# Kernel optimization log

Hardware: AMD Instinct MI355X
Metric: run time of the kernel (lower is better)

The kernel has to match this reference:

```python
import jax, jax.numpy as jnp
import numpy as np

B, T, I, H, K = 32, 1024, 512, 512, 2


def _causal_conv1d(x_bit, w_hik, b_h):
    # x_bit: [B, I, T]; left-pad K-1 zeros (ConstantPad1d((K-1, 0)))
    xp = jnp.pad(x_bit, ((0, 0), (0, 0), (K - 1, 0)))
    y = jax.lax.conv_general_dilated(
        xp, w_hik, window_strides=(1,), padding='VALID',
        dimension_numbers=('NCH', 'OIH', 'NCH'))  # [B, H, T]
    return y + b_h[None, :, None]


def setup_inputs() -> dict:
    key = jax.random.key(0)
    k1, k2, k3 = jax.random.split(key, 3)
    bound = 1.0 / np.sqrt(I * K)  # torch Conv1d default init scale
    return {
        'inputs': jax.random.normal(k1, (B, T, I), dtype=jnp.float32),
        'init_state': jnp.zeros((B, H), dtype=jnp.float32),
        'Wz': jax.random.uniform(k2, (H, I, K), jnp.float32, -bound, bound),
        'bz': jnp.zeros((H,), dtype=jnp.float32),
        'Wf': jax.random.uniform(k3, (H, I, K), jnp.float32, -bound, bound),
        'bf': jnp.zeros((H,), dtype=jnp.float32),
    }


def reference(inputs, init_state, Wz, bz, Wf, bf):
    # init_state is accepted but unused in the original forward (mode='f').
    x = inputs.transpose(0, 2, 1)                      # [B, I, T]
    raw_f = _causal_conv1d(x, Wf, bf).transpose(0, 2, 1)  # [B, T, H]
    raw_z = _causal_conv1d(x, Wz, bz).transpose(0, 2, 1)  # [B, T, H]

    log_f = jax.nn.log_sigmoid(raw_f)
    log_one_minus_f = jax.nn.log_sigmoid(-raw_f)
    log_z = jax.nn.log_sigmoid(raw_z)

    # recurrent_gates[t] = sum_{s>t} log_f[s]  (suffix sum of log_f over time, excluding t=0 shift)
    rg = log_f[:, 1:, :]                               # [B, T-1, H]
    cs = jnp.cumsum(rg, axis=1)
    rg = rg - cs + cs[:, -1:, :]
    rg = jnp.concatenate([rg, jnp.zeros((inputs.shape[0], 1, rg.shape[2]), dtype=rg.dtype)], axis=1)  # [B, T, H]

    log_hidden = jax.lax.cumlogsumexp(log_z + log_one_minus_f + rg, axis=1)
    hidden = jnp.exp(log_hidden - rg)
    return hidden
```

## Files before the change

kernel.cpp:

```cpp
#include <hip/hip_runtime.h>
#include <hip/hip_bf16.h>
#include <cstddef>
#include <cstdint>

#define B_  32
#define T_  1024
#define I_  512
#define H_  512
#define M_  (B_ * T_)
#define TP_ 1025

typedef __bf16 bf16x8  __attribute__((ext_vector_type(8)));
typedef float  floatx4 __attribute__((ext_vector_type(4)));
typedef unsigned short ushort8v __attribute__((ext_vector_type(8)));
typedef unsigned long long u64;

__device__ __forceinline__ unsigned short f2bf(float f) {
    uint32_t u = __float_as_uint(f);
    return (unsigned short)((u + 0x7FFFu + ((u >> 16) & 1u)) >> 16);
}
__device__ __forceinline__ float sigm(float x) {
    return __builtin_amdgcn_rcpf(1.f + __expf(-x));
}

#define GLL(src, dst) __builtin_amdgcn_global_load_lds( \
    (const __attribute__((address_space(1))) void*)(src), \
    (__attribute__((address_space(3))) void*)(dst), 16, 0, 0)

#define NB_BUILD 8200
#define NB_PACK  512
#define NB_ZERO  256

__global__ __launch_bounds__(256) void prep(const float* __restrict__ x,
                                            const float* __restrict__ Wf,
                                            const float* __restrict__ Wz,
                                            unsigned short* __restrict__ Ab2,
                                            unsigned short* __restrict__ Wq,
                                            uint4* __restrict__ HpubZ,
                                            uint32_t* __restrict__ tickets) {
    if (blockIdx.x < NB_BUILD) {
        int g = blockIdx.x * 256 + threadIdx.x;
        int idx8 = g << 3;
        int row = idx8 >> 9;
        int col = idx8 & 511;
        int b    = (int)((unsigned)row / TP_);
        int trow = row - b * TP_;
        ushort8v o = {0, 0, 0, 0, 0, 0, 0, 0};
        if (trow > 0) {
            const float* src = &x[((size_t)b * T_ + (trow - 1)) * I_ + col];
            float4 v0 = *(const float4*)src;
            float4 v1 = *(const float4*)(src + 4);
            o[0] = f2bf(v0.x); o[1] = f2bf(v0.y); o[2] = f2bf(v0.z); o[3] = f2bf(v0.w);
            o[4] = f2bf(v1.x); o[5] = f2bf(v1.y); o[6] = f2bf(v1.z); o[7] = f2bf(v1.w);
        }
        *(ushort8v*)&Ab2[(size_t)idx8] = o;
    } else if (blockIdx.x < NB_BUILD + NB_PACK) {
        int cid = (blockIdx.x - NB_BUILD) * 256 + threadIdx.x;
        int lane = cid & 63;
        int c    = (cid >> 6) & 3;
        int wn   = (cid >> 8) & 1;
        int ksub = (cid >> 9) & 31;
        int ni   = (cid >> 14) & 3;
        int gate = (cid >> 16) & 1;
        int n_col = ni * 128 + wn * 64 + c * 16 + (lane & 15);
        const float* G = gate ? Wz : Wf;
        ushort8v o;
        #pragma unroll
        for (int j = 0; j < 8; ++j) {
            int k   = ksub * 32 + (lane >> 4) * 8 + j;
            int tap = k >> 9;
            int i   = k & 511;
            o[j] = f2bf(G[n_col * (I_ * 2) + i * 2 + tap]);
        }
        *(ushort8v*)&Wq[(size_t)cid * 8] = o;
    } else {
        int g = (blockIdx.x - NB_BUILD - NB_PACK) * 256 + threadIdx.x;
        HpubZ[g] = make_uint4(0, 0, 0, 0);
        if (g < 256) tickets[g] = 0;
    }
}

__global__ __launch_bounds__(256, 3) void mfma_gemm_scan(
        const unsigned short* __restrict__ Ab2,
        const unsigned short* __restrict__ Wq,
        const float* __restrict__ biasF,
        const float* __restrict__ biasZ,
        float* __restrict__ out,
        u64* __restrict__ Hpub,
        uint32_t* __restrict__ tickets) {
    __shared__ unsigned short smem[12288];
    __shared__ uint32_t pos_s;

    const int tid = threadIdx.x;
    const int bid = blockIdx.x;
    const int x   = bid & 7;
    const int nh  = (bid >> 3) & 7;
    const int q   = bid >> 6;
    const int b   = ((q & 3) << 3) | x;
    const int chain = nh * 32 + b;
    if (tid == 0) pos_s = atomicAdd(&tickets[chain], 1u);
    __syncthreads();
    const int pos = (int)pos_s;
    const int h0  = nh * 64;
    const int browBase = b * TP_ + pos * 128;

    const int lane = tid & 63;
    const int wave = tid >> 6;
    const int wm   = wave >> 1;
    const int wh   = wave & 1;
    const int lm   = lane & 15, quad = lane >> 4;

    const int c0 = wave * 128 + lane;
    const int c1 = c0 + 64;
    const int r0 = c0 >> 2, q0 = (c0 & 3) ^ ((r0 >> 2) & 3);
    const int r1 = c1 >> 2, q1 = (c1 & 3) ^ ((r1 >> 2) & 3);

    const unsigned short* pA0 = Ab2 + (size_t)(browBase + r0) * 512 + q0 * 8;
    const unsigned short* pA1 = Ab2 + (size_t)(browBase + r1) * 512 + q1 * 8;

    const unsigned short* pBF = Wq + (size_t)(nh >> 1) * 131072
                                   + (nh & 1) * 2048 + wh * 1024 + lane * 8;

    int offA[4];
    #pragma unroll
    for (int r = 0; r < 4; ++r) {
        int ml = wm * 64 + r * 16 + lm;
        offA[r] = (4 * ml + (quad ^ ((ml >> 2) & 3))) * 8;
    }

    floatx4 accF[4][2] = {};
    floatx4 accZ[4][2] = {};
    bf16x8 bfA[2], bzA[2], bfB[2], bzB[2];

#define ISSUE_A(ksub, sA) do {                                          \
        const int aoff_ = (((ksub) >> 4) * 512) + (((ksub) & 15) * 32); \
        GLL(pA0 + aoff_, (sA) + wave * 1024);                           \
        GLL(pA1 + aoff_, (sA) + wave * 1024 + 512);                     \
    } while (0)

#define LOADB(ksub, BF, BZ) do {                                        \
        const unsigned short* pf_ = pBF + (ksub) * 4096;                \
        BF[0] = *(const bf16x8*)(pf_);                                  \
        BF[1] = *(const bf16x8*)(pf_ + 512);                            \
        BZ[0] = *(const bf16x8*)(pf_ + 524288);                         \
        BZ[1] = *(const bf16x8*)(pf_ + 524288 + 512);                   \
    } while (0)

#define MFMA16(AF, BF, BZ) do {                                         \
        __builtin_amdgcn_s_setprio(1);                                  \
        _Pragma("unroll")                                               \
        for (int r = 0; r < 4; ++r) {                                   \
            _Pragma("unroll")                                           \
            for (int c = 0; c < 2; ++c) {                               \
                accF[r][c] = __builtin_amdgcn_mfma_f32_16x16x32_bf16(   \
                                AF[r], BF[c], accF[r][c], 0, 0, 0);     \
                accZ[r][c] = __builtin_amdgcn_mfma_f32_16x16x32_bf16(   \
                                AF[r], BZ[c], accZ[r][c], 0, 0, 0);     \
            }                                                           \
        }                                                               \
        __builtin_amdgcn_s_setprio(0);                                  \
    } while (0)

#define RDA(slot, AF) do {                                              \
        _Pragma("unroll")                                               \
        for (int r = 0; r < 4; ++r)                                     \
            AF[r] = *(const bf16x8*)((slot) + offA[r]);                 \
    } while (0)

#define ROT() do { unsigned short* t_ = s0; s0 = s1; s1 = s2; s2 = t_; } while (0)

    unsigned short* s0 = smem;
    unsigned short* s1 = smem + 4096;
    unsigned short* s2 = smem + 8192;

    ISSUE_A(0, s0);
    LOADB(0, bfA, bzA);
    ISSUE_A(1, s1);

    {
        asm volatile("s_waitcnt vmcnt(2)");
        __builtin_amdgcn_s_barrier();
        asm volatile("" ::: "memory");
        bf16x8 af_[4];
        RDA(s0, af_);
        LOADB(1, bfB, bzB);
        ISSUE_A(2, s2);
        __builtin_amdgcn_sched_barrier(0);
        MFMA16(af_, bfA, bzA);
        ROT();
    }
    for (int p = 0; p < 14; ++p) {
        const int k1 = 2 * p + 1;
        {
            asm volatile("s_waitcnt vmcnt(2)");
            __builtin_amdgcn_s_barrier();
            asm volatile("" ::: "memory");
            bf16x8 af_[4];
            RDA(s0, af_);
            LOADB(k1 + 1, bfA, bzA);
            ISSUE_A(k1 + 2, s2);
            __builtin_amdgcn_sched_barrier(0);
            MFMA16(af_, bfB, bzB);
            ROT();
        }
        {
            asm volatile("s_waitcnt vmcnt(2)");
            __builtin_amdgcn_s_barrier();
            asm volatile("" ::: "memory");
            bf16x8 af_[4];
            RDA(s0, af_);
            LOADB(k1 + 2, bfB, bzB);
            ISSUE_A(k1 + 3, s2);
            __builtin_amdgcn_sched_barrier(0);
            MFMA16(af_, bfA, bzA);
            ROT();
        }
    }
    {
        asm volatile("s_waitcnt vmcnt(2)");
        __builtin_amdgcn_s_barrier();
        asm volatile("" ::: "memory");
        bf16x8 af_[4];
        RDA(s0, af_);
        LOADB(30, bfA, bzA);
        ISSUE_A(31, s2);
        __builtin_amdgcn_sched_barrier(0);
        MFMA16(af_, bfB, bzB);
        ROT();
    }
    {
        asm volatile("s_waitcnt vmcnt(2)");
        __builtin_amdgcn_s_barrier();
        asm volatile("" ::: "memory");
        bf16x8 af_[4];
        RDA(s0, af_);
        LOADB(31, bfB, bzB);
        __builtin_amdgcn_sched_barrier(0);
        MFMA16(af_, bfA, bzA);
        ROT();
    }
    {
        asm volatile("s_waitcnt vmcnt(0)");
        __builtin_amdgcn_s_barrier();
        asm volatile("" ::: "memory");
        bf16x8 af_[4];
        RDA(s0, af_);
        __builtin_amdgcn_sched_barrier(0);
        MFMA16(af_, bfB, bzB);
    }
#undef ISSUE_A
#undef LOADB
#undef MFMA16
#undef RDA
#undef ROT
    __syncthreads();

    float bfv[2], bzv[2];
    #pragma unroll
    for (int c = 0; c < 2; ++c) {
        int hc = h0 + wh * 32 + c * 16 + lm;
        bfv[c] = biasF[hc];
        bzv[c] = biasZ[hc];
    }

    float2* seg  = (float2*)smem;
    float*  hinL = (float*)&smem[8192];

    #pragma unroll
    for (int r = 0; r < 4; ++r) {
        const int sid = wm * 16 + r * 4 + quad;
        #pragma unroll
        for (int c = 0; c < 2; ++c) {
            float A = 1.f, C = 0.f;
            #pragma unroll
            for (int v = 0; v < 4; ++v) {
                float f = sigm(accF[r][c][v] + bfv[c]);
                float z = sigm(accZ[r][c][v] + bzv[c]);
                accF[r][c][v] = f;
                accZ[r][c][v] = z;
                A *= f;
                C = fmaf(f, C - z, z);
            }
            seg[sid * 64 + wh * 32 + c * 16 + lm] = make_float2(A, C);
        }
    }
    __syncthreads();

    if (tid < 64) {
        const int h = tid;
        float At = 1.f, Ct = 0.f;
        #pragma unroll 8
        for (int s = 0; s < 32; ++s) {
            float2 sc = seg[s * 64 + h];
            Ct = fmaf(sc.x, Ct, sc.y);
            At *= sc.x;
        }
        float Hin = 0.f;
        if (pos > 0) {
            u64* p = &Hpub[((size_t)(pos - 1) * 256 + chain) * 64 + h];
            u64 v;
            while (((v = atomicAdd(p, 0ull)) >> 32) == 0ull)
                __builtin_amdgcn_s_sleep(2);
            Hin = __uint_as_float((uint32_t)v);
        }
        if (pos < 7) {
            float Hout = fmaf(At, Hin, Ct);
            u64 pv = 0x100000000ull | (u64)__float_as_uint(Hout);
            atomicExch(&Hpub[((size_t)pos * 256 + chain) * 64 + h], pv);
        }
        float run = Hin;
        #pragma unroll 8
        for (int s = 0; s < 32; ++s) {
            hinL[s * 64 + h] = run;
            float2 sc = seg[s * 64 + h];
            run = fmaf(sc.x, run, sc.y);
        }
    }
    __syncthreads();

    const int rowBase = b * T_ + pos * 128;
    #pragma unroll
    for (int r = 0; r < 4; ++r) {
        const int sid = wm * 16 + r * 4 + quad;
        #pragma unroll
        for (int c = 0; c < 2; ++c) {
            const int hcl = wh * 32 + c * 16 + lm;
            float hs = hinL[sid * 64 + hcl];
            #pragma unroll
            for (int v = 0; v < 4; ++v) {
                float f = accF[r][c][v];
                float z = accZ[r][c][v];
                hs = fmaf(f, hs - z, z);
                const size_t row = (size_t)(rowBase + wm * 64 + r * 16 + quad * 4 + v);
                out[row * H_ + h0 + hcl] = hs;
            }
        }
    }
}

extern "C" void kernel_launch(void* const* d_in, const int* in_sizes, int n_in,
                              void* d_out, int out_size, void* d_ws, size_t ws_size,
                              hipStream_t stream) {
    const float* x  = (const float*)d_in[0];
    const float* Wz = (const float*)d_in[2];
    const float* bz = (const float*)d_in[3];
    const float* Wf = (const float*)d_in[4];
    const float* bf = (const float*)d_in[5];
    float* out = (float*)d_out;

    char* ws = (char*)d_ws;
    unsigned short* Ab2  = (unsigned short*)(ws);
    unsigned short* Wq   = (unsigned short*)(ws + (size_t)34 * 1024 * 1024);
    u64*            Hpub = (u64*)(ws + (size_t)36 * 1024 * 1024);
    uint32_t*       tkt  = (uint32_t*)(ws + (size_t)37 * 1024 * 1024);

    prep<<<NB_BUILD + NB_PACK + NB_ZERO, 256, 0, stream>>>(
        x, Wf, Wz, Ab2, Wq, (uint4*)Hpub, tkt);

    mfma_gemm_scan<<<2048, 256, 0, stream>>>(Ab2, Wq, bf, bz, out, Hpub, tkt);
}
```

Baseline: 203.2 us.

## Load A fragments directly from global into registers, dropping LDS staging

Replaces the triple-buffered global_load_lds staging of the A tile, along with its per-step barriers and swizzled LDS reads, with direct per-wave global loads of A fragments into registers. These are double-buffered alongside the B loads. This removes LDS traffic and block-wide barriers from the K loop. In exchange each A row is loaded by both wh waves (duplicate global traffic), the loads are less coalesced, and there is more register pressure and exposed latency.

After: 288.6 us. +42.0%, slower.

```diff
diff --git a/kernel.cpp b/kernel.cpp
--- a/kernel.cpp
+++ b/kernel.cpp
@@ -22,10 +22,6 @@
 __device__ __forceinline__ float sigm(float x) {
     return __builtin_amdgcn_rcpf(1.f + __expf(-x));
 }
-
-#define GLL(src, dst) __builtin_amdgcn_global_load_lds( \
-    (const __attribute__((address_space(1))) void*)(src), \
-    (__attribute__((address_space(3))) void*)(dst), 16, 0, 0)
 
 #define NB_BUILD 8200
 #define NB_PACK  512
@@ -110,32 +106,22 @@
     const int wh   = wave & 1;
     const int lm   = lane & 15, quad = lane >> 4;
 
-    const int c0 = wave * 128 + lane;
-    const int c1 = c0 + 64;
-    const int r0 = c0 >> 2, q0 = (c0 & 3) ^ ((r0 >> 2) & 3);
-    const int r1 = c1 >> 2, q1 = (c1 & 3) ^ ((r1 >> 2) & 3);
-
-    const unsigned short* pA0 = Ab2 + (size_t)(browBase + r0) * 512 + q0 * 8;
-    const unsigned short* pA1 = Ab2 + (size_t)(browBase + r1) * 512 + q1 * 8;
+    const unsigned short* pA_base =
+        Ab2 + (size_t)(browBase + wm * 64 + lm) * 512 + quad * 8;
 
     const unsigned short* pBF = Wq + (size_t)(nh >> 1) * 131072
                                    + (nh & 1) * 2048 + wh * 1024 + lane * 8;
 
-    int offA[4];
-    #pragma unroll
-    for (int r = 0; r < 4; ++r) {
-        int ml = wm * 64 + r * 16 + lm;
-        offA[r] = (4 * ml + (quad ^ ((ml >> 2) & 3))) * 8;
-    }
-
     floatx4 accF[4][2] = {};
     floatx4 accZ[4][2] = {};
-    bf16x8 bfA[2], bzA[2], bfB[2], bzB[2];
-
-#define ISSUE_A(ksub, sA) do {                                          \
-        const int aoff_ = (((ksub) >> 4) * 512) + (((ksub) & 15) * 32); \
-        GLL(pA0 + aoff_, (sA) + wave * 1024);                           \
-        GLL(pA1 + aoff_, (sA) + wave * 1024 + 512);                     \
+    bf16x8 aA[4], aB[4], bfA[2], bzA[2], bfB[2], bzB[2];
+
+#define LOADA(ksub, AF) do {                                            \
+        const unsigned short* pa_ = pA_base + (ksub) * 32;              \
+        AF[0] = *(const bf16x8*)(pa_);                                  \
+        AF[1] = *(const bf16x8*)(pa_ + 8192);                           \
+        AF[2] = *(const bf16x8*)(pa_ + 16384);                          \
+        AF[3] = *(const bf16x8*)(pa_ + 24576);                          \
     } while (0)
 
 #define LOADB(ksub, BF, BZ) do {                                        \
@@ -161,99 +147,32 @@
         __builtin_amdgcn_s_setprio(0);                                  \
     } while (0)
 
-#define RDA(slot, AF) do {                                              \
-        _Pragma("unroll")                                               \
-        for (int r = 0; r < 4; ++r)                                     \
-            AF[r] = *(const bf16x8*)((slot) + offA[r]);                 \
-    } while (0)
-
-#define ROT() do { unsigned short* t_ = s0; s0 = s1; s1 = s2; s2 = t_; } while (0)
-
-    unsigned short* s0 = smem;
-    unsigned short* s1 = smem + 4096;
-    unsigned short* s2 = smem + 8192;
-
-    ISSUE_A(0, s0);
+    LOADA(0, aA);
     LOADB(0, bfA, bzA);
-    ISSUE_A(1, s1);
-
-    {
-        asm volatile("s_waitcnt vmcnt(2)");
-        __builtin_amdgcn_s_barrier();
-        asm volatile("" ::: "memory");
-        bf16x8 af_[4];
-        RDA(s0, af_);
-        LOADB(1, bfB, bzB);
-        ISSUE_A(2, s2);
-        __builtin_amdgcn_sched_barrier(0);
-        MFMA16(af_, bfA, bzA);
-        ROT();
-    }
-    for (int p = 0; p < 14; ++p) {
-        const int k1 = 2 * p + 1;
-        {
-            asm volatile("s_waitcnt vmcnt(2)");
-            __builtin_amdgcn_s_barrier();
-            asm volatile("" ::: "memory");
-            bf16x8 af_[4];
-            RDA(s0, af_);
-            LOADB(k1 + 1, bfA, bzA);
-            ISSUE_A(k1 + 2, s2);
-            __builtin_amdgcn_sched_barrier(0);
-            MFMA16(af_, bfB, bzB);
-            ROT();
-        }
-        {
-            asm volatile("s_waitcnt vmcnt(2)");
-            __builtin_amdgcn_s_barrier();
-            asm volatile("" ::: "memory");
-            bf16x8 af_[4];
-            RDA(s0, af_);
-            LOADB(k1 + 2, bfB, bzB);
-            ISSUE_A(k1 + 3, s2);
-            __builtin_amdgcn_sched_barrier(0);
-            MFMA16(af_, bfA, bzA);
-            ROT();
-        }
-    }
-    {
-        asm volatile("s_waitcnt vmcnt(2)");
-        __builtin_amdgcn_s_barrier();
-        asm volatile("" ::: "memory");
-        bf16x8 af_[4];
-        RDA(s0, af_);
-        LOADB(30, bfA, bzA);
-        ISSUE_A(31, s2);
-        __builtin_amdgcn_sched_barrier(0);
-        MFMA16(af_, bfB, bzB);
-        ROT();
-    }
-    {
-        asm volatile("s_waitcnt vmcnt(2)");
-        __builtin_amdgcn_s_barrier();
-        asm volatile("" ::: "memory");
-        bf16x8 af_[4];
-        RDA(s0, af_);
-        LOADB(31, bfB, bzB);
-        __builtin_amdgcn_sched_barrier(0);
-        MFMA16(af_, bfA, bzA);
-        ROT();
-    }
-    {
-        asm volatile("s_waitcnt vmcnt(0)");
-        __builtin_amdgcn_s_barrier();
-        asm volatile("" ::: "memory");
-        bf16x8 af_[4];
-        RDA(s0, af_);
-        __builtin_amdgcn_sched_barrier(0);
-        MFMA16(af_, bfB, bzB);
-    }
-#undef ISSUE_A
+
+    #pragma unroll 1
+    for (int p = 0; p < 15; ++p) {
+        const int k = 2 * p;
+        LOADA(k + 1, aB);
+        LOADB(k + 1, bfB, bzB);
+        __builtin_amdgcn_sched_barrier(0);
+        MFMA16(aA, bfA, bzA);
+        __builtin_amdgcn_sched_barrier(0);
+        LOADA(k + 2, aA);
+        LOADB(k + 2, bfA, bzA);
+        __builtin_amdgcn_sched_barrier(0);
+        MFMA16(aB, bfB, bzB);
+        __builtin_amdgcn_sched_barrier(0);
+    }
+    LOADA(31, aB);
+    LOADB(31, bfB, bzB);
+    __builtin_amdgcn_sched_barrier(0);
+    MFMA16(aA, bfA, bzA);
+    __builtin_amdgcn_sched_barrier(0);
+    MFMA16(aB, bfB, bzB);
+#undef LOADA
 #undef LOADB
 #undef MFMA16
-#undef RDA
-#undef ROT
-    __syncthreads();
 
     float bfv[2], bzv[2];
     #pragma unroll
```
